# Kernel tuning notes

Hardware: AMD Instinct MI355X
Metric: run time of the kernel (lower is better)

The kernel has to match this reference:

```python
import jax, jax.numpy as jnp
import numpy as np

ALPHA = 0.5  # init kwarg alpha
V, F, E, B = 500_000, 2_000_000, 8_000_000, 128


def setup_inputs() -> dict:
    key = jax.random.key(0)
    k = jax.random.split(key, 8)
    variable_prediction = jax.random.uniform(k[0], (V, 1), jnp.float32)  # sigmoid-like preds in (0,1)
    degree_loss = jax.random.uniform(k[1], (V,), jnp.float32) + 0.5      # positive per-variable weights
    var_idx = jax.random.randint(k[2], (E,), 0, V, dtype=jnp.int32)
    fun_idx = jax.random.randint(k[3], (E,), 0, F, dtype=jnp.int32)
    graph_map = jnp.stack([var_idx, fun_idx])                            # [2, E]
    # literal polarity +/-1 (sparse mask values in the torch code)
    edge_feature = jnp.where(jax.random.normal(k[4], (E, 1)) >= 0, 1.0, -1.0).astype(jnp.float32)
    batch_variable_map = jnp.sort(jax.random.randint(k[5], (V,), 0, B, dtype=jnp.int32))
    batch_function_map = jnp.sort(jax.random.randint(k[6], (F,), 0, B, dtype=jnp.int32))
    return {
        "variable_prediction": variable_prediction,
        "degree_loss": degree_loss,
        "label": jnp.ones((B,), jnp.float32),
        "graph_map": graph_map,
        "batch_variable_map": batch_variable_map,
        "batch_function_map": batch_function_map,
        "edge_feature": edge_feature,
        "meta_data": jnp.zeros((1,), jnp.float32),
        "global_step": jnp.array([100.0], jnp.float32),
        "eps": jnp.array([1e-10], jnp.float32),
        "max_coeff": jnp.array([10.0], jnp.float32),
        "loss_sharpness": 5,
    }


def reference(variable_prediction, degree_loss, label, graph_map, batch_variable_map,
              batch_function_map, edge_feature, meta_data, global_step, eps, max_coeff,
              loss_sharpness):
    function_num = batch_function_map.shape[0]
    coeff = jnp.minimum(global_step[0] ** ALPHA, max_coeff[0])
    var_idx = graph_map[0]
    fun_idx = graph_map[1]
    ef = edge_feature[:, 0]                                             # [E]
    # mm(signed_variable_mask_transpose, variable_prediction) == gather * polarity
    edge_values = ef * variable_prediction[var_idx, 0] + (1.0 - ef) * 0.5  # [E]
    weights = jnp.exp(coeff * edge_values)                              # [E]
    # mm(function_mask, .) == segment-sum over clauses
    nominator = jax.ops.segment_sum(weights * edge_values, fun_idx, num_segments=function_num)
    denominator = jax.ops.segment_sum(weights, fun_idx, num_segments=function_num)
    clause_value = denominator / jnp.maximum(nominator, eps[0])         # [F]
    clause_value = 1.0 + (clause_value - 1.0) ** loss_sharpness
    # degree_loss branch: sparse.mm chain == gather then clause segment-sum
    temp_loss = jax.ops.segment_sum(ef * degree_loss[var_idx], fun_idx, num_segments=function_num)
    clause_value = temp_loss * clause_value
    # safe_log: clamp to >=0, floor at eps, log, then mean
    safe = jnp.log(jnp.maximum(jnp.clip(clause_value, 0.0), eps[0]))
    return jnp.mean(safe)
```

## Files before the change

### kernel.cpp

```cpp
#include <hip/hip_runtime.h>
#include <math.h>


#define THREADS 256
#define S_LOG2  11
#define S_FUN   2048
#define K_MAX   1024
#define TILE    8192
#define ITEMS   (TILE / THREADS)
#define QUADS   (ITEMS / 4)
#define DSCALE  1024.0f
#define DRECIP  (1.0f / 1024.0f)
#define TSCALE  65536.0f
#define TRECIP  (1.0f / 65536.0f)

typedef unsigned uint4n __attribute__((ext_vector_type(4)));
typedef float    float4n __attribute__((ext_vector_type(4)));
typedef float    float2n __attribute__((ext_vector_type(2)));

__global__ void __launch_bounds__(THREADS)
bin_edges(const int* __restrict__ gmap,
          const float* __restrict__ ef,
          const float* __restrict__ vp,
          const float* __restrict__ dl,
          float2n* __restrict__ vpdl,
          unsigned* __restrict__ gcounts,
          unsigned* __restrict__ records,
          int E, int V, int K, int cap, int tiles) {
    __shared__ unsigned hist[K_MAX];
    __shared__ unsigned offs[K_MAX];
    __shared__ unsigned staging[TILE];

    if (blockIdx.x >= (unsigned)tiles) {
        int q = (blockIdx.x - tiles) * THREADS + threadIdx.x;
        if (q * 4 + 3 < V) {
            float4n p4 = __builtin_nontemporal_load((const float4n*)vp + q);
            float4n d4 = __builtin_nontemporal_load((const float4n*)dl + q);
            #pragma unroll
            for (int c = 0; c < 4; ++c) {
                float2n t; t.x = p4[c]; t.y = d4[c];
                __builtin_nontemporal_store(t, vpdl + q * 4 + c);
            }
        } else {
            for (int c = 0; c < 4; ++c) {
                int i = q * 4 + c;
                if (i < V) { float2n t; t.x = vp[i]; t.y = dl[i]; vpdl[i] = t; }
            }
        }
        return;
    }

    unsigned rec[ITEMS];
    unsigned bp[ITEMS];

    int base = blockIdx.x * TILE;
    int n = min(TILE, E - base);
    bool full = (n == TILE);

    for (int i = threadIdx.x; i < K; i += THREADS) hist[i] = 0u;
    __syncthreads();

    const unsigned* funp = (const unsigned*)(gmap + E) + base;
    const unsigned* varp = (const unsigned*)gmap + base;
    const float*    efp  = ef + base;

    #pragma unroll
    for (int k = 0; k < QUADS; ++k) {
        int q = k * THREADS + threadIdx.x;
        if (full || q * 4 + 3 < n) {
            uint4n  f4 = __builtin_nontemporal_load((const uint4n*)funp + q);
            uint4n  v4 = __builtin_nontemporal_load((const uint4n*)varp + q);
            float4n e4 = __builtin_nontemporal_load((const float4n*)efp + q);
            #pragma unroll
            for (int c = 0; c < 4; ++c) {
                unsigned f = f4[c], v = v4[c];
                float    e = e4[c];
                unsigned b = f >> S_LOG2;
                rec[k * 4 + c] = ((f & (S_FUN - 1)) << 20) |
                                 ((e < 0.0f ? 1u : 0u) << 19) | v;
                unsigned pos = atomicAdd(&hist[b], 1u);
                bp[k * 4 + c] = (b << 13) | pos;
            }
        } else {
            #pragma unroll
            for (int c = 0; c < 4; ++c) {
                int j = q * 4 + c;
                if (j < n) {
                    unsigned f = funp[j], v = varp[j];
                    float    e = efp[j];
                    unsigned b = f >> S_LOG2;
                    rec[k * 4 + c] = ((f & (S_FUN - 1)) << 20) |
                                     ((e < 0.0f ? 1u : 0u) << 19) | v;
                    unsigned pos = atomicAdd(&hist[b], 1u);
                    bp[k * 4 + c] = (b << 13) | pos;
                } else bp[k * 4 + c] = 0xFFFFFFFFu;
            }
        }
    }
    __syncthreads();

    {
        unsigned* wred = staging;
        int t4 = threadIdx.x * 4;
        unsigned a0 = (t4 + 0 < K) ? hist[t4 + 0] : 0u;
        unsigned a1 = (t4 + 1 < K) ? hist[t4 + 1] : 0u;
        unsigned a2 = (t4 + 2 < K) ? hist[t4 + 2] : 0u;
        unsigned a3 = (t4 + 3 < K) ? hist[t4 + 3] : 0u;
        unsigned s = a0 + a1 + a2 + a3;
        unsigned sc = s;
        int lane = threadIdx.x & 63, wid = threadIdx.x >> 6;
        #pragma unroll
        for (int d = 1; d < 64; d <<= 1) {
            unsigned t = __shfl_up(sc, d, 64);
            if (lane >= d) sc += t;
        }
        if (lane == 63) wred[wid] = sc;
        __syncthreads();
        unsigned wb = 0;
        for (int w = 0; w < wid; ++w) wb += wred[w];
        unsigned ex = wb + sc - s;
        if (t4 + 0 < K) { offs[t4 + 0] = ex; ex += a0; }
        if (t4 + 1 < K) { offs[t4 + 1] = ex; ex += a1; }
        if (t4 + 2 < K) { offs[t4 + 2] = ex; ex += a2; }
        if (t4 + 3 < K) { offs[t4 + 3] = ex; ex += a3; }
    }
    __syncthreads();

    for (int b = threadIdx.x; b < K; b += THREADS) {
        unsigned h = hist[b];
        if (h) hist[b] = atomicAdd(&gcounts[b], h) - offs[b];
    }
    __syncthreads();

    #pragma unroll
    for (int k = 0; k < ITEMS; ++k) {
        unsigned m = bp[k];
        if (m != 0xFFFFFFFFu)
            staging[offs[m >> 13] + (m & 0x1FFFu)] = rec[k];
    }
    __syncthreads();

    for (int j = threadIdx.x; j < n; j += THREADS) {
        unsigned r = staging[j];
        int lo = 0, hi = K - 1;
        while (lo < hi) {
            int mid = (lo + hi + 1) >> 1;
            if (offs[mid] <= (unsigned)j) lo = mid; else hi = mid - 1;
        }
        unsigned dst = hist[lo] + (unsigned)j;
        if (dst < (unsigned)cap)
            __builtin_nontemporal_store(r, &records[(size_t)lo * cap + dst]);
    }
}

__global__ void __launch_bounds__(THREADS)
bucket_accum(const float2n* __restrict__ vpdl,
             const unsigned* __restrict__ gcounts,
             const unsigned* __restrict__ records,
             const float* __restrict__ gs,
             const float* __restrict__ mc,
             const float* __restrict__ eps_p,
             const int* __restrict__ ls_p,
             double* __restrict__ partials,
             int F, int cap) {
    __shared__ float accN[S_FUN];
    __shared__ unsigned long long accDT[S_FUN];
    __shared__ float red[THREADS / 64];

    int b = blockIdx.x;
    for (int i = threadIdx.x; i < S_FUN; i += THREADS) {
        accN[i] = 0.0f; accDT[i] = 0ull;
    }
    __syncthreads();

    float coeff = fminf(sqrtf(gs[0]), mc[0]);
    unsigned cnt = gcounts[b];
    if (cnt > (unsigned)cap) cnt = (unsigned)cap;
    const unsigned* rec = records + (size_t)b * cap;

    #define PROC1(R_, T_) {                                            \
        float e_ = ((R_) >> 19) & 1u ? -1.0f : 1.0f;                   \
        unsigned s_ = (R_) >> 20;                                      \
        float ev_ = e_ * (T_).x + (1.0f - e_) * 0.5f;                  \
        float w_ = __expf(coeff * ev_);                                \
        unsigned dq_ = (unsigned)(w_ * DSCALE + 0.5f);                 \
        int tq_ = (int)rintf(e_ * (T_).y * TSCALE);                    \
        atomicAdd(&accN[s_], w_ * ev_);                                \
        atomicAdd(&accDT[s_],                                          \
            ((unsigned long long)(long long)tq_ << 32) + dq_); }

    unsigned n4 = cnt >> 2;
    for (unsigned j = threadIdx.x; j < n4; j += 2 * THREADS) {
        unsigned j2 = j + THREADS;
        uint4n ra = __builtin_nontemporal_load((const uint4n*)rec + j);
        if (j2 < n4) {
            uint4n rb = __builtin_nontemporal_load((const uint4n*)rec + j2);
            unsigned r[8] = {ra[0], ra[1], ra[2], ra[3], rb[0], rb[1], rb[2], rb[3]};
            float2n t[8];
            #pragma unroll
            for (int c = 0; c < 8; ++c) t[c] = vpdl[r[c] & 0x7FFFFu];
            #pragma unroll
            for (int c = 0; c < 8; ++c) PROC1(r[c], t[c]);
        } else {
            unsigned r[4] = {ra[0], ra[1], ra[2], ra[3]};
            float2n t[4];
            #pragma unroll
            for (int c = 0; c < 4; ++c) t[c] = vpdl[r[c] & 0x7FFFFu];
            #pragma unroll
            for (int c = 0; c < 4; ++c) PROC1(r[c], t[c]);
        }
    }
    for (unsigned j = (n4 << 2) + threadIdx.x; j < cnt; j += THREADS) {
        unsigned r = rec[j];
        float2n t = vpdl[r & 0x7FFFFu];
        PROC1(r, t);
    }
    #undef PROC1
    __syncthreads();

    float epsv = eps_p[0];
    int   ls   = ls_p[0];
    float local = 0.0f;
    int fbase = b << S_LOG2;
    for (int i = threadIdx.x; i < S_FUN; i += THREADS) {
        int fg = fbase + i;
        if (fg < F) {
            unsigned long long nd = accDT[i];
            float D = (float)(unsigned)(nd & 0xFFFFFFFFull) * DRECIP;
            float T = (float)(int)(nd >> 32) * TRECIP;
            float cv = D / fmaxf(accN[i], epsv);
            float d = cv - 1.0f;
            float p = 1.0f;
            for (int k = 0; k < ls; ++k) p *= d;
            cv = T * (1.0f + p);
            local += __logf(fmaxf(cv, epsv));
        }
    }
    #pragma unroll
    for (int off = 32; off > 0; off >>= 1)
        local += __shfl_down(local, off, 64);
    int lane = threadIdx.x & 63, wid = threadIdx.x >> 6;
    if (lane == 0) red[wid] = local;
    __syncthreads();
    if (threadIdx.x == 0) {
        float s = 0.0f;
        #pragma unroll
        for (int w = 0; w < THREADS / 64; ++w) s += red[w];
        partials[b] = (double)s;
    }
}

__global__ void final_reduce(const double* __restrict__ partials, int nparts,
                             float* __restrict__ out, int F) {
    __shared__ double sm[THREADS];
    double local = 0.0;
    for (int i = threadIdx.x; i < nparts; i += blockDim.x) local += partials[i];
    sm[threadIdx.x] = local;
    __syncthreads();
    for (int s = blockDim.x / 2; s > 0; s >>= 1) {
        if ((int)threadIdx.x < s) sm[threadIdx.x] += sm[threadIdx.x + s];
        __syncthreads();
    }
    if (threadIdx.x == 0) out[0] = (float)(sm[0] / (double)F);
}

extern "C" void kernel_launch(void* const* d_in, const int* in_sizes, int n_in,
                              void* d_out, int out_size, void* d_ws, size_t ws_size,
                              hipStream_t stream) {
    const float* vp   = (const float*)d_in[0];
    const float* dl   = (const float*)d_in[1];
    const int*   gmap = (const int*)d_in[3];
    const float* ef   = (const float*)d_in[6];
    const float* gs   = (const float*)d_in[8];
    const float* eps  = (const float*)d_in[9];
    const float* mc   = (const float*)d_in[10];
    const int*   ls   = (const int*)d_in[11];

    const int V = in_sizes[0];
    const int F = in_sizes[5];
    const int E = in_sizes[6];
    const int K = (F + S_FUN - 1) / S_FUN;

    size_t off = ((size_t)K * sizeof(unsigned) + 15) & ~(size_t)15;
    unsigned* gcounts = (unsigned*)d_ws;
    double* partials = (double*)((char*)d_ws + off);
    off = (off + (size_t)K * sizeof(double) + 15) & ~(size_t)15;
    float2n* vpdl = (float2n*)((char*)d_ws + off);
    off = (off + (size_t)V * sizeof(float2n) + 15) & ~(size_t)15;

    long long cap = (ws_size > off)
        ? (long long)((ws_size - off) / ((size_t)K * sizeof(unsigned))) : 4;
    if (cap > 16384) cap = 16384;
    cap &= ~3LL;
    if (cap < 4) cap = 4;

    unsigned* records = (unsigned*)((char*)d_ws + off);

    hipMemsetAsync(gcounts, 0, (size_t)K * sizeof(unsigned), stream);

    int tiles = (E + TILE - 1) / TILE;
    int fblocks = (V + THREADS * 4 - 1) / (THREADS * 4);
    bin_edges<<<tiles + fblocks, THREADS, 0, stream>>>(
        gmap, ef, vp, dl, vpdl, gcounts, records, E, V, K, (int)cap, tiles);

    bucket_accum<<<K, THREADS, 0, stream>>>(vpdl, gcounts, records,
                                            gs, mc, eps, ls, partials,
                                            F, (int)cap);

    final_reduce<<<1, THREADS, 0, stream>>>(partials, K, (float*)d_out, F);
}
```

Measured before the change: 277.6 us.

## Counting-sort bucket records by function in LDS, then reduce per function without atomics

Replaces the per-edge LDS float and 64-bit packed fixed-point atomics in bucket_accum with a local counting sort. Records are histogrammed by function, prefix-scanned and scattered into a shared staging array. Each thread then walks one function's edges, gathers vpdl and accumulates N, D and T in registers. This removes atomic contention and the fixed-point quantisation, at the cost of an extra pass, a smaller record cap (9216), load imbalance across functions with different degrees, and serialised dependent gathers per thread.

```diff
diff --git a/kernel.cpp b/kernel.cpp
--- a/kernel.cpp
+++ b/kernel.cpp
@@ -9,10 +9,8 @@
 #define TILE    8192
 #define ITEMS   (TILE / THREADS)
 #define QUADS   (ITEMS / 4)
-#define DSCALE  1024.0f
-#define DRECIP  (1.0f / 1024.0f)
-#define TSCALE  65536.0f
-#define TRECIP  (1.0f / 65536.0f)
+#define SCAP    9216
+#define MAXQ    (SCAP / 4 / THREADS)
 
 typedef unsigned uint4n __attribute__((ext_vector_type(4)));
 typedef float    float4n __attribute__((ext_vector_type(4)));
@@ -163,78 +161,103 @@
              const int* __restrict__ ls_p,
              double* __restrict__ partials,
              int F, int cap) {
-    __shared__ float accN[S_FUN];
-    __shared__ unsigned long long accDT[S_FUN];
+    __shared__ unsigned fhist[S_FUN];
+    __shared__ unsigned foffs[S_FUN];
+    __shared__ unsigned stag[SCAP];
+    __shared__ unsigned wred[THREADS / 64];
     __shared__ float red[THREADS / 64];
 
     int b = blockIdx.x;
-    for (int i = threadIdx.x; i < S_FUN; i += THREADS) {
-        accN[i] = 0.0f; accDT[i] = 0ull;
-    }
-    __syncthreads();
-
-    float coeff = fminf(sqrtf(gs[0]), mc[0]);
+    for (int i = threadIdx.x; i < S_FUN; i += THREADS) fhist[i] = 0u;
+    __syncthreads();
+
     unsigned cnt = gcounts[b];
     if (cnt > (unsigned)cap) cnt = (unsigned)cap;
+    if (cnt > SCAP) cnt = SCAP;
     const unsigned* rec = records + (size_t)b * cap;
 
-    #define PROC1(R_, T_) {                                            \
-        float e_ = ((R_) >> 19) & 1u ? -1.0f : 1.0f;                   \
-        unsigned s_ = (R_) >> 20;                                      \
-        float ev_ = e_ * (T_).x + (1.0f - e_) * 0.5f;                  \
-        float w_ = __expf(coeff * ev_);                                \
-        unsigned dq_ = (unsigned)(w_ * DSCALE + 0.5f);                 \
-        int tq_ = (int)rintf(e_ * (T_).y * TSCALE);                    \
-        atomicAdd(&accN[s_], w_ * ev_);                                \
-        atomicAdd(&accDT[s_],                                          \
-            ((unsigned long long)(long long)tq_ << 32) + dq_); }
-
-    unsigned n4 = cnt >> 2;
-    for (unsigned j = threadIdx.x; j < n4; j += 2 * THREADS) {
-        unsigned j2 = j + THREADS;
-        uint4n ra = __builtin_nontemporal_load((const uint4n*)rec + j);
-        if (j2 < n4) {
-            uint4n rb = __builtin_nontemporal_load((const uint4n*)rec + j2);
-            unsigned r[8] = {ra[0], ra[1], ra[2], ra[3], rb[0], rb[1], rb[2], rb[3]};
-            float2n t[8];
-            #pragma unroll
-            for (int c = 0; c < 8; ++c) t[c] = vpdl[r[c] & 0x7FFFFu];
-            #pragma unroll
-            for (int c = 0; c < 8; ++c) PROC1(r[c], t[c]);
-        } else {
-            unsigned r[4] = {ra[0], ra[1], ra[2], ra[3]};
-            float2n t[4];
-            #pragma unroll
-            for (int c = 0; c < 4; ++c) t[c] = vpdl[r[c] & 0x7FFFFu];
-            #pragma unroll
-            for (int c = 0; c < 4; ++c) PROC1(r[c], t[c]);
-        }
-    }
-    for (unsigned j = (n4 << 2) + threadIdx.x; j < cnt; j += THREADS) {
-        unsigned r = rec[j];
-        float2n t = vpdl[r & 0x7FFFFu];
-        PROC1(r, t);
-    }
-    #undef PROC1
-    __syncthreads();
-
+    uint4n r4[MAXQ];
+    unsigned ps[MAXQ * 4];
+    unsigned cnt4 = cnt >> 2;
+    #pragma unroll
+    for (int k = 0; k < MAXQ; ++k) {
+        unsigned q = threadIdx.x + k * THREADS;
+        if (q < cnt4) {
+            r4[k] = __builtin_nontemporal_load((const uint4n*)rec + q);
+            #pragma unroll
+            for (int c = 0; c < 4; ++c)
+                ps[k * 4 + c] = atomicAdd(&fhist[r4[k][c] >> 20], 1u);
+        }
+    }
+    unsigned tr = 0u, tp = 0u; bool thave = false;
+    for (unsigned j = (cnt4 << 2) + threadIdx.x; j < cnt; j += THREADS) {
+        tr = rec[j];
+        tp = atomicAdd(&fhist[tr >> 20], 1u);
+        thave = true;
+    }
+    __syncthreads();
+
+    {
+        int t8 = threadIdx.x * 8;
+        unsigned a[8], s = 0;
+        #pragma unroll
+        for (int c = 0; c < 8; ++c) { a[c] = fhist[t8 + c]; s += a[c]; }
+        unsigned sc = s;
+        int lane = threadIdx.x & 63, wid = threadIdx.x >> 6;
+        #pragma unroll
+        for (int d = 1; d < 64; d <<= 1) {
+            unsigned t = __shfl_up(sc, d, 64);
+            if (lane >= d) sc += t;
+        }
+        if (lane == 63) wred[wid] = sc;
+        __syncthreads();
+        unsigned wb = 0;
+        for (int w = 0; w < wid; ++w) wb += wred[w];
+        unsigned ex = wb + sc - s;
+        #pragma unroll
+        for (int c = 0; c < 8; ++c) { foffs[t8 + c] = ex; ex += a[c]; }
+    }
+    __syncthreads();
+
+    #pragma unroll
+    for (int k = 0; k < MAXQ; ++k) {
+        unsigned q = threadIdx.x + k * THREADS;
+        if (q < cnt4) {
+            #pragma unroll
+            for (int c = 0; c < 4; ++c) {
+                unsigned r = r4[k][c];
+                stag[foffs[r >> 20] + ps[k * 4 + c]] = r;
+            }
+        }
+    }
+    if (thave) stag[foffs[tr >> 20] + tp] = tr;
+    __syncthreads();
+
+    float coeff = fminf(sqrtf(gs[0]), mc[0]);
     float epsv = eps_p[0];
     int   ls   = ls_p[0];
     float local = 0.0f;
     int fbase = b << S_LOG2;
-    for (int i = threadIdx.x; i < S_FUN; i += THREADS) {
-        int fg = fbase + i;
-        if (fg < F) {
-            unsigned long long nd = accDT[i];
-            float D = (float)(unsigned)(nd & 0xFFFFFFFFull) * DRECIP;
-            float T = (float)(int)(nd >> 32) * TRECIP;
-            float cv = D / fmaxf(accN[i], epsv);
-            float d = cv - 1.0f;
-            float p = 1.0f;
-            for (int k = 0; k < ls; ++k) p *= d;
-            cv = T * (1.0f + p);
-            local += __logf(fmaxf(cv, epsv));
-        }
+    for (int fl = threadIdx.x; fl < S_FUN; fl += THREADS) {
+        int fg = fbase + fl;
+        if (fg >= F) break;
+        unsigned start = foffs[fl];
+        unsigned deg   = fhist[fl];
+        float N = 0.0f, D = 0.0f, T = 0.0f;
+        for (unsigned i = 0; i < deg; ++i) {
+            unsigned r = stag[start + i];
+            float e = (r >> 19) & 1u ? -1.0f : 1.0f;
+            float2n t = vpdl[r & 0x7FFFFu];
+            float ev = e * t.x + (1.0f - e) * 0.5f;
+            float w = __expf(coeff * ev);
+            N += w * ev; D += w; T += e * t.y;
+        }
+        float cv = D / fmaxf(N, epsv);
+        float d = cv - 1.0f;
+        float p = 1.0f;
+        for (int k = 0; k < ls; ++k) p *= d;
+        cv = T * (1.0f + p);
+        local += __logf(fmaxf(cv, epsv));
     }
     #pragma unroll
     for (int off = 32; off > 0; off >>= 1)
@@ -290,7 +313,7 @@
 
     long long cap = (ws_size > off)
         ? (long long)((ws_size - off) / ((size_t)K * sizeof(unsigned))) : 4;
-    if (cap > 16384) cap = 16384;
+    if (cap > SCAP) cap = SCAP;
     cap &= ~3LL;
     if (cap < 4) cap = 4;
 
```

Measured after the change: 285.2 us. 1.03x slower.

## Fuse memset, binning, bucket accumulation and final reduce into one cooperative kernel

Applied to the files above, without the earlier changes.

Replaces the memset plus three separate kernel launches with a single persistent cooperative kernel that uses grid-wide syncs between phases. Tiles and buckets are processed in grid-stride loops, and shared memory is aliased across phases. The aim is to remove launch overhead and inter-kernel gaps. In exchange it pays grid.sync costs and accepts lower occupancy per phase, since the grid is capped at the number of blocks that fit on the device at once.

```diff
diff --git a/kernel.cpp b/kernel.cpp
--- a/kernel.cpp
+++ b/kernel.cpp
@@ -1,5 +1,8 @@
 #include <hip/hip_runtime.h>
+#include <hip/hip_cooperative_groups.h>
 #include <math.h>
+
+namespace cg = cooperative_groups;
 
 
 #define THREADS 256
@@ -18,250 +21,252 @@
 typedef float    float4n __attribute__((ext_vector_type(4)));
 typedef float    float2n __attribute__((ext_vector_type(2)));
 
-__global__ void __launch_bounds__(THREADS)
-bin_edges(const int* __restrict__ gmap,
-          const float* __restrict__ ef,
-          const float* __restrict__ vp,
-          const float* __restrict__ dl,
-          float2n* __restrict__ vpdl,
-          unsigned* __restrict__ gcounts,
-          unsigned* __restrict__ records,
-          int E, int V, int K, int cap, int tiles) {
-    __shared__ unsigned hist[K_MAX];
-    __shared__ unsigned offs[K_MAX];
-    __shared__ unsigned staging[TILE];
-
-    if (blockIdx.x >= (unsigned)tiles) {
-        int q = (blockIdx.x - tiles) * THREADS + threadIdx.x;
-        if (q * 4 + 3 < V) {
-            float4n p4 = __builtin_nontemporal_load((const float4n*)vp + q);
-            float4n d4 = __builtin_nontemporal_load((const float4n*)dl + q);
-            #pragma unroll
-            for (int c = 0; c < 4; ++c) {
-                float2n t; t.x = p4[c]; t.y = d4[c];
-                __builtin_nontemporal_store(t, vpdl + q * 4 + c);
-            }
-        } else {
-            for (int c = 0; c < 4; ++c) {
-                int i = q * 4 + c;
-                if (i < V) { float2n t; t.x = vp[i]; t.y = dl[i]; vpdl[i] = t; }
-            }
-        }
-        return;
-    }
-
-    unsigned rec[ITEMS];
-    unsigned bp[ITEMS];
-
-    int base = blockIdx.x * TILE;
-    int n = min(TILE, E - base);
-    bool full = (n == TILE);
-
-    for (int i = threadIdx.x; i < K; i += THREADS) hist[i] = 0u;
-    __syncthreads();
-
-    const unsigned* funp = (const unsigned*)(gmap + E) + base;
-    const unsigned* varp = (const unsigned*)gmap + base;
-    const float*    efp  = ef + base;
-
-    #pragma unroll
-    for (int k = 0; k < QUADS; ++k) {
-        int q = k * THREADS + threadIdx.x;
-        if (full || q * 4 + 3 < n) {
-            uint4n  f4 = __builtin_nontemporal_load((const uint4n*)funp + q);
-            uint4n  v4 = __builtin_nontemporal_load((const uint4n*)varp + q);
-            float4n e4 = __builtin_nontemporal_load((const float4n*)efp + q);
-            #pragma unroll
-            for (int c = 0; c < 4; ++c) {
-                unsigned f = f4[c], v = v4[c];
-                float    e = e4[c];
-                unsigned b = f >> S_LOG2;
-                rec[k * 4 + c] = ((f & (S_FUN - 1)) << 20) |
-                                 ((e < 0.0f ? 1u : 0u) << 19) | v;
-                unsigned pos = atomicAdd(&hist[b], 1u);
-                bp[k * 4 + c] = (b << 13) | pos;
-            }
-        } else {
-            #pragma unroll
-            for (int c = 0; c < 4; ++c) {
-                int j = q * 4 + c;
-                if (j < n) {
-                    unsigned f = funp[j], v = varp[j];
-                    float    e = efp[j];
+__global__ void __launch_bounds__(THREADS, 4)
+fused_all(const int* __restrict__ gmap, const float* __restrict__ ef,
+          const float* __restrict__ vp, const float* __restrict__ dl,
+          float2n* __restrict__ vpdl, unsigned* __restrict__ gcounts,
+          unsigned* __restrict__ records, double* __restrict__ partials,
+          float* __restrict__ out,
+          const float* __restrict__ gs, const float* __restrict__ mc,
+          const float* __restrict__ eps_p, const int* __restrict__ ls_p,
+          int E, int V, int F, int K, int cap, int tiles, int fblocks) {
+    cg::grid_group grid = cg::this_grid();
+    __shared__ __attribute__((aligned(16))) unsigned char smem[40960];
+    unsigned* hist    = (unsigned*)smem;
+    unsigned* offs    = hist + K_MAX;
+    unsigned* staging = offs + K_MAX;
+    unsigned long long* accDT = (unsigned long long*)smem;
+    float* accN = (float*)(smem + 16384);
+    float* red  = (float*)(smem + 16384 + 8192);
+    double* smd = (double*)smem;
+
+    for (int i = blockIdx.x * THREADS + threadIdx.x; i < K;
+         i += gridDim.x * THREADS)
+        gcounts[i] = 0u;
+    grid.sync();
+
+    for (int vt = blockIdx.x; vt < tiles + fblocks; vt += gridDim.x) {
+        if (vt >= tiles) {
+            int q = (vt - tiles) * THREADS + threadIdx.x;
+            if (q * 4 + 3 < V) {
+                float4n p4 = __builtin_nontemporal_load((const float4n*)vp + q);
+                float4n d4 = __builtin_nontemporal_load((const float4n*)dl + q);
+                #pragma unroll
+                for (int c = 0; c < 4; ++c) {
+                    float2n t; t.x = p4[c]; t.y = d4[c];
+                    __builtin_nontemporal_store(t, vpdl + q * 4 + c);
+                }
+            } else {
+                for (int c = 0; c < 4; ++c) {
+                    int i = q * 4 + c;
+                    if (i < V) { float2n t; t.x = vp[i]; t.y = dl[i]; vpdl[i] = t; }
+                }
+            }
+            continue;
+        }
+
+        unsigned rec[ITEMS];
+        unsigned bp[ITEMS];
+
+        int base = vt * TILE;
+        int n = min(TILE, E - base);
+        bool full = (n == TILE);
+
+        for (int i = threadIdx.x; i < K; i += THREADS) hist[i] = 0u;
+        __syncthreads();
+
+        const unsigned* funp = (const unsigned*)(gmap + E) + base;
+        const unsigned* varp = (const unsigned*)gmap + base;
+        const float*    efp  = ef + base;
+
+        #pragma unroll
+        for (int k = 0; k < QUADS; ++k) {
+            int q = k * THREADS + threadIdx.x;
+            if (full || q * 4 + 3 < n) {
+                uint4n  f4 = __builtin_nontemporal_load((const uint4n*)funp + q);
+                uint4n  v4 = __builtin_nontemporal_load((const uint4n*)varp + q);
+                float4n e4 = __builtin_nontemporal_load((const float4n*)efp + q);
+                #pragma unroll
+                for (int c = 0; c < 4; ++c) {
+                    unsigned f = f4[c], v = v4[c];
+                    float    e = e4[c];
                     unsigned b = f >> S_LOG2;
                     rec[k * 4 + c] = ((f & (S_FUN - 1)) << 20) |
                                      ((e < 0.0f ? 1u : 0u) << 19) | v;
                     unsigned pos = atomicAdd(&hist[b], 1u);
                     bp[k * 4 + c] = (b << 13) | pos;
-                } else bp[k * 4 + c] = 0xFFFFFFFFu;
-            }
-        }
+                }
+            } else {
+                #pragma unroll
+                for (int c = 0; c < 4; ++c) {
+                    int j = q * 4 + c;
+                    if (j < n) {
+                        unsigned f = funp[j], v = varp[j];
+                        float    e = efp[j];
+                        unsigned b = f >> S_LOG2;
+                        rec[k * 4 + c] = ((f & (S_FUN - 1)) << 20) |
+                                         ((e < 0.0f ? 1u : 0u) << 19) | v;
+                        unsigned pos = atomicAdd(&hist[b], 1u);
+                        bp[k * 4 + c] = (b << 13) | pos;
+                    } else bp[k * 4 + c] = 0xFFFFFFFFu;
+                }
+            }
+        }
+        __syncthreads();
+
+        {
+            unsigned* wred = staging;
+            int t4 = threadIdx.x * 4;
+            unsigned a0 = (t4 + 0 < K) ? hist[t4 + 0] : 0u;
+            unsigned a1 = (t4 + 1 < K) ? hist[t4 + 1] : 0u;
+            unsigned a2 = (t4 + 2 < K) ? hist[t4 + 2] : 0u;
+            unsigned a3 = (t4 + 3 < K) ? hist[t4 + 3] : 0u;
+            unsigned s = a0 + a1 + a2 + a3;
+            unsigned sc = s;
+            int lane = threadIdx.x & 63, wid = threadIdx.x >> 6;
+            #pragma unroll
+            for (int d = 1; d < 64; d <<= 1) {
+                unsigned t = __shfl_up(sc, d, 64);
+                if (lane >= d) sc += t;
+            }
+            if (lane == 63) wred[wid] = sc;
+            __syncthreads();
+            unsigned wb = 0;
+            for (int w = 0; w < wid; ++w) wb += wred[w];
+            unsigned ex = wb + sc - s;
+            if (t4 + 0 < K) { offs[t4 + 0] = ex; ex += a0; }
+            if (t4 + 1 < K) { offs[t4 + 1] = ex; ex += a1; }
+            if (t4 + 2 < K) { offs[t4 + 2] = ex; ex += a2; }
+            if (t4 + 3 < K) { offs[t4 + 3] = ex; ex += a3; }
+        }
+        __syncthreads();
+
+        for (int b = threadIdx.x; b < K; b += THREADS) {
+            unsigned h = hist[b];
+            if (h) hist[b] = atomicAdd(&gcounts[b], h) - offs[b];
+        }
+        __syncthreads();
+
+        #pragma unroll
+        for (int k = 0; k < ITEMS; ++k) {
+            unsigned m = bp[k];
+            if (m != 0xFFFFFFFFu)
+                staging[offs[m >> 13] + (m & 0x1FFFu)] = rec[k];
+        }
+        __syncthreads();
+
+        for (int j = threadIdx.x; j < n; j += THREADS) {
+            unsigned r = staging[j];
+            int lo = 0, hi = K - 1;
+            while (lo < hi) {
+                int mid = (lo + hi + 1) >> 1;
+                if (offs[mid] <= (unsigned)j) lo = mid; else hi = mid - 1;
+            }
+            unsigned dst = hist[lo] + (unsigned)j;
+            if (dst < (unsigned)cap)
+                __builtin_nontemporal_store(r, &records[(size_t)lo * cap + dst]);
+        }
+        __syncthreads();
     }
-    __syncthreads();
-
-    {
-        unsigned* wred = staging;
-        int t4 = threadIdx.x * 4;
-        unsigned a0 = (t4 + 0 < K) ? hist[t4 + 0] : 0u;
-        unsigned a1 = (t4 + 1 < K) ? hist[t4 + 1] : 0u;
-        unsigned a2 = (t4 + 2 < K) ? hist[t4 + 2] : 0u;
-        unsigned a3 = (t4 + 3 < K) ? hist[t4 + 3] : 0u;
-        unsigned s = a0 + a1 + a2 + a3;
-        unsigned sc = s;
-        int lane = threadIdx.x & 63, wid = threadIdx.x >> 6;
-        #pragma unroll
-        for (int d = 1; d < 64; d <<= 1) {
-            unsigned t = __shfl_up(sc, d, 64);
-            if (lane >= d) sc += t;
-        }
-        if (lane == 63) wred[wid] = sc;
-        __syncthreads();
-        unsigned wb = 0;
-        for (int w = 0; w < wid; ++w) wb += wred[w];
-        unsigned ex = wb + sc - s;
-        if (t4 + 0 < K) { offs[t4 + 0] = ex; ex += a0; }
-        if (t4 + 1 < K) { offs[t4 + 1] = ex; ex += a1; }
-        if (t4 + 2 < K) { offs[t4 + 2] = ex; ex += a2; }
-        if (t4 + 3 < K) { offs[t4 + 3] = ex; ex += a3; }
-    }
-    __syncthreads();
-
-    for (int b = threadIdx.x; b < K; b += THREADS) {
-        unsigned h = hist[b];
-        if (h) hist[b] = atomicAdd(&gcounts[b], h) - offs[b];
-    }
-    __syncthreads();
-
-    #pragma unroll
-    for (int k = 0; k < ITEMS; ++k) {
-        unsigned m = bp[k];
-        if (m != 0xFFFFFFFFu)
-            staging[offs[m >> 13] + (m & 0x1FFFu)] = rec[k];
-    }
-    __syncthreads();
-
-    for (int j = threadIdx.x; j < n; j += THREADS) {
-        unsigned r = staging[j];
-        int lo = 0, hi = K - 1;
-        while (lo < hi) {
-            int mid = (lo + hi + 1) >> 1;
-            if (offs[mid] <= (unsigned)j) lo = mid; else hi = mid - 1;
-        }
-        unsigned dst = hist[lo] + (unsigned)j;
-        if (dst < (unsigned)cap)
-            __builtin_nontemporal_store(r, &records[(size_t)lo * cap + dst]);
-    }
-}
-
-__global__ void __launch_bounds__(THREADS)
-bucket_accum(const float2n* __restrict__ vpdl,
-             const unsigned* __restrict__ gcounts,
-             const unsigned* __restrict__ records,
-             const float* __restrict__ gs,
-             const float* __restrict__ mc,
-             const float* __restrict__ eps_p,
-             const int* __restrict__ ls_p,
-             double* __restrict__ partials,
-             int F, int cap) {
-    __shared__ float accN[S_FUN];
-    __shared__ unsigned long long accDT[S_FUN];
-    __shared__ float red[THREADS / 64];
-
-    int b = blockIdx.x;
-    for (int i = threadIdx.x; i < S_FUN; i += THREADS) {
-        accN[i] = 0.0f; accDT[i] = 0ull;
-    }
-    __syncthreads();
+    grid.sync();
 
     float coeff = fminf(sqrtf(gs[0]), mc[0]);
-    unsigned cnt = gcounts[b];
-    if (cnt > (unsigned)cap) cnt = (unsigned)cap;
-    const unsigned* rec = records + (size_t)b * cap;
-
-    #define PROC1(R_, T_) {                                            \
-        float e_ = ((R_) >> 19) & 1u ? -1.0f : 1.0f;                   \
-        unsigned s_ = (R_) >> 20;                                      \
-        float ev_ = e_ * (T_).x + (1.0f - e_) * 0.5f;                  \
-        float w_ = __expf(coeff * ev_);                                \
-        unsigned dq_ = (unsigned)(w_ * DSCALE + 0.5f);                 \
-        int tq_ = (int)rintf(e_ * (T_).y * TSCALE);                    \
-        atomicAdd(&accN[s_], w_ * ev_);                                \
-        atomicAdd(&accDT[s_],                                          \
-            ((unsigned long long)(long long)tq_ << 32) + dq_); }
-
-    unsigned n4 = cnt >> 2;
-    for (unsigned j = threadIdx.x; j < n4; j += 2 * THREADS) {
-        unsigned j2 = j + THREADS;
-        uint4n ra = __builtin_nontemporal_load((const uint4n*)rec + j);
-        if (j2 < n4) {
-            uint4n rb = __builtin_nontemporal_load((const uint4n*)rec + j2);
-            unsigned r[8] = {ra[0], ra[1], ra[2], ra[3], rb[0], rb[1], rb[2], rb[3]};
-            float2n t[8];
-            #pragma unroll
-            for (int c = 0; c < 8; ++c) t[c] = vpdl[r[c] & 0x7FFFFu];
-            #pragma unroll
-            for (int c = 0; c < 8; ++c) PROC1(r[c], t[c]);
-        } else {
-            unsigned r[4] = {ra[0], ra[1], ra[2], ra[3]};
-            float2n t[4];
-            #pragma unroll
-            for (int c = 0; c < 4; ++c) t[c] = vpdl[r[c] & 0x7FFFFu];
-            #pragma unroll
-            for (int c = 0; c < 4; ++c) PROC1(r[c], t[c]);
-        }
-    }
-    for (unsigned j = (n4 << 2) + threadIdx.x; j < cnt; j += THREADS) {
-        unsigned r = rec[j];
-        float2n t = vpdl[r & 0x7FFFFu];
-        PROC1(r, t);
-    }
-    #undef PROC1
-    __syncthreads();
-
     float epsv = eps_p[0];
     int   ls   = ls_p[0];
-    float local = 0.0f;
-    int fbase = b << S_LOG2;
-    for (int i = threadIdx.x; i < S_FUN; i += THREADS) {
-        int fg = fbase + i;
-        if (fg < F) {
-            unsigned long long nd = accDT[i];
-            float D = (float)(unsigned)(nd & 0xFFFFFFFFull) * DRECIP;
-            float T = (float)(int)(nd >> 32) * TRECIP;
-            float cv = D / fmaxf(accN[i], epsv);
-            float d = cv - 1.0f;
-            float p = 1.0f;
-            for (int k = 0; k < ls; ++k) p *= d;
-            cv = T * (1.0f + p);
-            local += __logf(fmaxf(cv, epsv));
-        }
+    for (int b = blockIdx.x; b < K; b += gridDim.x) {
+        for (int i = threadIdx.x; i < S_FUN; i += THREADS) {
+            accN[i] = 0.0f; accDT[i] = 0ull;
+        }
+        __syncthreads();
+
+        unsigned cnt = gcounts[b];
+        if (cnt > (unsigned)cap) cnt = (unsigned)cap;
+        const unsigned* rec = records + (size_t)b * cap;
+
+        #define PROC1(R_, T_) {                                            \
+            float e_ = ((R_) >> 19) & 1u ? -1.0f : 1.0f;                   \
+            unsigned s_ = (R_) >> 20;                                      \
+            float ev_ = e_ * (T_).x + (1.0f - e_) * 0.5f;                  \
+            float w_ = __expf(coeff * ev_);                                \
+            unsigned dq_ = (unsigned)(w_ * DSCALE + 0.5f);                 \
+            int tq_ = (int)rintf(e_ * (T_).y * TSCALE);                    \
+            atomicAdd(&accN[s_], w_ * ev_);                                \
+            atomicAdd(&accDT[s_],                                          \
+                ((unsigned long long)(long long)tq_ << 32) + dq_); }
+
+        unsigned n4 = cnt >> 2;
+        for (unsigned j = threadIdx.x; j < n4; j += 2 * THREADS) {
+            unsigned j2 = j + THREADS;
+            uint4n ra = __builtin_nontemporal_load((const uint4n*)rec + j);
+            if (j2 < n4) {
+                uint4n rb = __builtin_nontemporal_load((const uint4n*)rec + j2);
+                unsigned r[8] = {ra[0], ra[1], ra[2], ra[3],
+                                 rb[0], rb[1], rb[2], rb[3]};
+                float2n t[8];
+                #pragma unroll
+                for (int c = 0; c < 8; ++c) t[c] = vpdl[r[c] & 0x7FFFFu];
+                #pragma unroll
+                for (int c = 0; c < 8; ++c) PROC1(r[c], t[c]);
+            } else {
+                unsigned r[4] = {ra[0], ra[1], ra[2], ra[3]};
+                float2n t[4];
+                #pragma unroll
+                for (int c = 0; c < 4; ++c) t[c] = vpdl[r[c] & 0x7FFFFu];
+                #pragma unroll
+                for (int c = 0; c < 4; ++c) PROC1(r[c], t[c]);
+            }
+        }
+        for (unsigned j = (n4 << 2) + threadIdx.x; j < cnt; j += THREADS) {
+            unsigned r = rec[j];
+            float2n t = vpdl[r & 0x7FFFFu];
+            PROC1(r, t);
+        }
+        #undef PROC1
+        __syncthreads();
+
+        float local = 0.0f;
+        int fbase = b << S_LOG2;
+        for (int i = threadIdx.x; i < S_FUN; i += THREADS) {
+            int fg = fbase + i;
+            if (fg < F) {
+                unsigned long long nd = accDT[i];
+                float D = (float)(unsigned)(nd & 0xFFFFFFFFull) * DRECIP;
+                float T = (float)(int)(nd >> 32) * TRECIP;
+                float cv = D / fmaxf(accN[i], epsv);
+                float d = cv - 1.0f;
+                float p = 1.0f;
+                for (int k = 0; k < ls; ++k) p *= d;
+                cv = T * (1.0f + p);
+                local += __logf(fmaxf(cv, epsv));
+            }
+        }
+        #pragma unroll
+        for (int off = 32; off > 0; off >>= 1)
+            local += __shfl_down(local, off, 64);
+        int lane = threadIdx.x & 63, wid = threadIdx.x >> 6;
+        if (lane == 0) red[wid] = local;
+        __syncthreads();
+        if (threadIdx.x == 0) {
+            float s = 0.0f;
+            #pragma unroll
+            for (int w = 0; w < THREADS / 64; ++w) s += red[w];
+            partials[b] = (double)s;
+        }
+        __syncthreads();
     }
-    #pragma unroll
-    for (int off = 32; off > 0; off >>= 1)
-        local += __shfl_down(local, off, 64);
-    int lane = threadIdx.x & 63, wid = threadIdx.x >> 6;
-    if (lane == 0) red[wid] = local;
-    __syncthreads();
-    if (threadIdx.x == 0) {
-        float s = 0.0f;
-        #pragma unroll
-        for (int w = 0; w < THREADS / 64; ++w) s += red[w];
-        partials[b] = (double)s;
+    grid.sync();
+
+    if (blockIdx.x == 0) {
+        double local = 0.0;
+        for (int i = threadIdx.x; i < K; i += THREADS) local += partials[i];
+        smd[threadIdx.x] = local;
+        __syncthreads();
+        for (int s = THREADS / 2; s > 0; s >>= 1) {
+            if ((int)threadIdx.x < s) smd[threadIdx.x] += smd[threadIdx.x + s];
+            __syncthreads();
+        }
+        if (threadIdx.x == 0) out[0] = (float)(smd[0] / (double)F);
     }
-}
-
-__global__ void final_reduce(const double* __restrict__ partials, int nparts,
-                             float* __restrict__ out, int F) {
-    __shared__ double sm[THREADS];
-    double local = 0.0;
-    for (int i = threadIdx.x; i < nparts; i += blockDim.x) local += partials[i];
-    sm[threadIdx.x] = local;
-    __syncthreads();
-    for (int s = blockDim.x / 2; s > 0; s >>= 1) {
-        if ((int)threadIdx.x < s) sm[threadIdx.x] += sm[threadIdx.x + s];
-        __syncthreads();
-    }
-    if (threadIdx.x == 0) out[0] = (float)(sm[0] / (double)F);
 }
 
 extern "C" void kernel_launch(void* const* d_in, const int* in_sizes, int n_in,
@@ -276,10 +281,10 @@
     const float* mc   = (const float*)d_in[10];
     const int*   ls   = (const int*)d_in[11];
 
-    const int V = in_sizes[0];
-    const int F = in_sizes[5];
-    const int E = in_sizes[6];
-    const int K = (F + S_FUN - 1) / S_FUN;
+    int V = in_sizes[0];
+    int F = in_sizes[5];
+    int E = in_sizes[6];
+    int K = (F + S_FUN - 1) / S_FUN;
 
     size_t off = ((size_t)K * sizeof(unsigned) + 15) & ~(size_t)15;
     unsigned* gcounts = (unsigned*)d_ws;
@@ -288,24 +293,32 @@
     float2n* vpdl = (float2n*)((char*)d_ws + off);
     off = (off + (size_t)V * sizeof(float2n) + 15) & ~(size_t)15;
 
-    long long cap = (ws_size > off)
+    long long cap64 = (ws_size > off)
         ? (long long)((ws_size - off) / ((size_t)K * sizeof(unsigned))) : 4;
-    if (cap > 16384) cap = 16384;
-    cap &= ~3LL;
-    if (cap < 4) cap = 4;
+    if (cap64 > 16384) cap64 = 16384;
+    cap64 &= ~3LL;
+    if (cap64 < 4) cap64 = 4;
+    int cap = (int)cap64;
 
     unsigned* records = (unsigned*)((char*)d_ws + off);
-
-    hipMemsetAsync(gcounts, 0, (size_t)K * sizeof(unsigned), stream);
+    float* out = (float*)d_out;
 
     int tiles = (E + TILE - 1) / TILE;
     int fblocks = (V + THREADS * 4 - 1) / (THREADS * 4);
-    bin_edges<<<tiles + fblocks, THREADS, 0, stream>>>(
-        gmap, ef, vp, dl, vpdl, gcounts, records, E, V, K, (int)cap, tiles);
-
-    bucket_accum<<<K, THREADS, 0, stream>>>(vpdl, gcounts, records,
-                                            gs, mc, eps, ls, partials,
-                                            F, (int)cap);
-
-    final_reduce<<<1, THREADS, 0, stream>>>(partials, K, (float*)d_out, F);
+
+    int per_cu = 0;
+    hipOccupancyMaxActiveBlocksPerMultiprocessor(&per_cu, fused_all, THREADS, 0);
+    if (per_cu < 1) per_cu = 1;
+    int grid = per_cu * 256;
+    if (grid > 1024) grid = 1024;
+
+    void* args[] = {
+        (void*)&gmap, (void*)&ef, (void*)&vp, (void*)&dl, (void*)&vpdl,
+        (void*)&gcounts, (void*)&records, (void*)&partials, (void*)&out,
+        (void*)&gs, (void*)&mc, (void*)&eps, (void*)&ls,
+        (void*)&E, (void*)&V, (void*)&F, (void*)&K, (void*)&cap,
+        (void*)&tiles, (void*)&fblocks
+    };
+    hipLaunchCooperativeKernel(reinterpret_cast<void*>(fused_all),
+                               dim3(grid), dim3(THREADS), args, 0, stream);
 }
```

New measurement: 455.4 us. 1.64x slower.
